# Optimization experiments

Hardware: AMD Instinct MI355X
Metric: run time of the kernel (lower is better)

The kernel has to match this reference:

```python
import jax, jax.numpy as jnp
import numpy as np

N, E = 100000, 1600000
F_IN, F_HID, F_OUT = 64, 64, 16


def setup_inputs() -> dict:
    key = jax.random.key(0)
    ks = jax.random.split(key, 10)
    def g(k, shape):
        return jax.random.normal(k, shape, dtype=jnp.float32) * 0.05
    return {
        "x": jax.random.normal(ks[0], (N, F_IN), dtype=jnp.float32),
        "adj": jax.random.randint(ks[1], (2, E), 0, N, dtype=jnp.int32),
        # ChebConv K=2 params: per-order weights [in, out] + shared bias
        "W1_0": g(ks[2], (F_IN, F_HID)), "W1_1": g(ks[3], (F_IN, F_HID)),
        "b1": jnp.zeros((F_HID,), jnp.float32),
        "Wx_0": g(ks[4], (F_HID, F_HID)), "Wx_1": g(ks[5], (F_HID, F_HID)),
        "bx": jnp.zeros((F_HID,), jnp.float32),
        "W2_0": g(ks[6], (F_HID, F_OUT)), "W2_1": g(ks[7], (F_HID, F_OUT)),
        "b2": jnp.zeros((F_OUT,), jnp.float32),
    }


def _cheb(x, row, col, w, W0, W1, b):
    # K=2 Chebyshev conv: Tx0 = x, Tx1 = L_hat @ x (sparse propagate)
    n = x.shape[0]
    tx1 = jax.ops.segment_sum(w[:, None] * x[col], row, num_segments=n)
    return x @ W0 + tx1 @ W1 + b


def reference(x, adj, W1_0, W1_1, b1, Wx_0, Wx_1, bx, W2_0, W2_1, b2):
    row, col = adj[0], adj[1]
    n = x.shape[0]
    # sym-normalized Laplacian scaled by 2/lambda_max (=1): diagonal cancels,
    # off-diagonal weight = -deg^{-1/2}[row] * deg^{-1/2}[col]
    deg = jax.ops.segment_sum(jnp.ones(adj.shape[1], x.dtype), row, num_segments=n)
    dis = jnp.where(deg > 0, jax.lax.rsqrt(jnp.maximum(deg, 1e-12)), 0.0)
    w = -dis[row] * dis[col]
    h = jax.nn.relu(_cheb(x, row, col, w, W1_0, W1_1, b1))
    # dropout is identity in eval mode
    h = jax.nn.relu(_cheb(h, row, col, w, Wx_0, Wx_1, bx))
    return _cheb(h, row, col, w, W2_0, W2_1, b2)
```

## Files before the change

kernel.cpp:

```cpp
#include <hip/hip_runtime.h>
#include <hip/hip_bf16.h>


#define EPB 4096

typedef __attribute__((ext_vector_type(8))) short bf16x8;
typedef __attribute__((ext_vector_type(4))) float f32x4;

__device__ __forceinline__ float bf2f(unsigned short u) {
    unsigned int x = ((unsigned int)u) << 16;
    return __uint_as_float(x);
}
__device__ __forceinline__ unsigned short f2bf(float f) {
    unsigned int b = __float_as_uint(f);
    unsigned int r = (b + 0x7FFF + ((b >> 16) & 1)) >> 16;
    return (unsigned short)r;
}

__global__ __launch_bounds__(256) void zero_ints(int* __restrict__ p, int n) {
    int i = blockIdx.x * 256 + threadIdx.x;
    if (i < n) p[i] = 0;
}

__global__ __launch_bounds__(256) void bucket_count(const int* __restrict__ row,
                                                    int* __restrict__ bcnt,
                                                    int e, int nbk) {
    __shared__ int bh[512];
    int tid = threadIdx.x;
    for (int j = tid; j < nbk; j += 256) bh[j] = 0;
    __syncthreads();
    int base = blockIdx.x * EPB;
#pragma unroll
    for (int k = 0; k < EPB / 256; ++k) {
        int i = base + k * 256 + tid;
        if (i < e) atomicAdd(&bh[row[i] >> 8], 1);
    }
    __syncthreads();
    for (int j = tid; j < nbk; j += 256) {
        int c = bh[j];
        if (c) atomicAdd(&bcnt[j], c);
    }
}

__global__ __launch_bounds__(256) void bucket_scan(const int* __restrict__ bcnt,
                                                   int* __restrict__ bbase,
                                                   int* __restrict__ bcursor,
                                                   int* __restrict__ off,
                                                   int nbk, int n, int e) {
    __shared__ int sa[512], sb[512];
    int tid = threadIdx.x;
    for (int j = tid; j < 512; j += 256) sa[j] = (j < nbk) ? bcnt[j] : 0;
    __syncthreads();
    int* in = sa;
    int* out = sb;
    for (int d = 1; d < 512; d <<= 1) {
        for (int j = tid; j < 512; j += 256)
            out[j] = in[j] + ((j >= d) ? in[j - d] : 0);
        __syncthreads();
        int* t = in; in = out; out = t;
    }
    for (int j = tid; j < nbk; j += 256) {
        int incl = in[j];
        int excl = incl - bcnt[j];
        bbase[j] = excl;
        bcursor[j] = excl;
        if (j == nbk - 1) bbase[nbk] = incl;
    }
    if (tid == 0) off[n] = e;
}

__global__ __launch_bounds__(256) void bucket_scatter(const int* __restrict__ row,
                                                      const int* __restrict__ col,
                                                      int* __restrict__ bcursor,
                                                      int* __restrict__ packed,
                                                      int e, int nbk) {
    __shared__ int bh[512];
    __shared__ int bbase[512];
    __shared__ int bcur[512];
    int tid = threadIdx.x;
    for (int j = tid; j < nbk; j += 256) { bh[j] = 0; bcur[j] = 0; }
    __syncthreads();
    int base = blockIdx.x * EPB;
#pragma unroll
    for (int k = 0; k < EPB / 256; ++k) {
        int i = base + k * 256 + tid;
        if (i < e) atomicAdd(&bh[row[i] >> 8], 1);
    }
    __syncthreads();
    for (int j = tid; j < nbk; j += 256) {
        int c = bh[j];
        bbase[j] = c ? atomicAdd(&bcursor[j], c) : 0;
    }
    __syncthreads();
#pragma unroll
    for (int k = 0; k < EPB / 256; ++k) {
        int i = base + k * 256 + tid;
        if (i < e) {
            int r = row[i];
            int b = r >> 8;
            int slot = bbase[b] + atomicAdd(&bcur[b], 1);
            packed[slot] = ((r & 255) << 17) | col[i];
        }
    }
}

__global__ __launch_bounds__(256) void bucket_build(const int* __restrict__ packed,
                                                    const int* __restrict__ bbase,
                                                    int* __restrict__ off,
                                                    float* __restrict__ dis,
                                                    int* __restrict__ csr, int n) {
    __shared__ int rcnt[256];
    __shared__ int sa[256], sb[256];
    int tid = threadIdx.x;
    int b = blockIdx.x;
    int ebase = bbase[b], eend = bbase[b + 1];
    rcnt[tid] = 0;
    __syncthreads();
    for (int e = ebase + tid; e < eend; e += 256)
        atomicAdd(&rcnt[packed[e] >> 17], 1);
    __syncthreads();
    sa[tid] = rcnt[tid];
    __syncthreads();
    int* in = sa;
    int* out = sb;
    for (int d = 1; d < 256; d <<= 1) {
        out[tid] = in[tid] + ((tid >= d) ? in[tid - d] : 0);
        __syncthreads();
        int* t = in; in = out; out = t;
    }
    int grow = b * 256 + tid;
    int c = rcnt[tid];
    int excl = in[tid] - c;
    if (grow < n) {
        off[grow] = ebase + excl;
        dis[grow] = (c > 0) ? rsqrtf((float)c) : 0.0f;
    }
    out[tid] = excl;
    __syncthreads();
    for (int e = ebase + tid; e < eend; e += 256) {
        int p = packed[e];
        int lr = p >> 17;
        int pos = atomicAdd(&out[lr], 1);
        csr[ebase + pos] = p & 0x1FFFF;
    }
}


__global__ __launch_bounds__(256) void scale_xy(const float* __restrict__ x,
                                                const float* __restrict__ dis,
                                                unsigned short* __restrict__ y,
                                                unsigned short* __restrict__ xb, int n) {
    int id = blockIdx.x * 256 + threadIdx.x;
    if (id < n * 16) {
        int r = id >> 4;
        float d = dis[r];
        float4 v = ((const float4*)x)[id];
        ushort4 o = {f2bf(v.x * d), f2bf(v.y * d), f2bf(v.z * d), f2bf(v.w * d)};
        ((ushort4*)y)[id] = o;
        ushort4 xo = {f2bf(v.x), f2bf(v.y), f2bf(v.z), f2bf(v.w)};
        ((ushort4*)xb)[id] = xo;
    }
}


__global__ __launch_bounds__(256) void aggregate(const unsigned short* __restrict__ y,
                                                 const int* __restrict__ csr,
                                                 const int* __restrict__ off,
                                                 const float* __restrict__ dis,
                                                 unsigned short* __restrict__ tx, int n) {
    int tid = threadIdx.x;
    int r = blockIdx.x * 16 + (tid >> 4);
    if (r >= n) return;
    int q = tid & 15;
    int s0 = off[r], e1 = off[r + 1];
    const ushort4* Y = (const ushort4*)y;
    float ax = 0.f, ay = 0.f, az = 0.f, aw = 0.f;
    int t = s0;
    for (; t + 8 <= e1; t += 8) {
        int c0 = csr[t], c1 = csr[t + 1], c2 = csr[t + 2], c3 = csr[t + 3];
        int c4 = csr[t + 4], c5 = csr[t + 5], c6 = csr[t + 6], c7 = csr[t + 7];
        ushort4 v0 = Y[(size_t)c0 * 16 + q];
        ushort4 v1 = Y[(size_t)c1 * 16 + q];
        ushort4 v2 = Y[(size_t)c2 * 16 + q];
        ushort4 v3 = Y[(size_t)c3 * 16 + q];
        ushort4 v4 = Y[(size_t)c4 * 16 + q];
        ushort4 v5 = Y[(size_t)c5 * 16 + q];
        ushort4 v6 = Y[(size_t)c6 * 16 + q];
        ushort4 v7 = Y[(size_t)c7 * 16 + q];
        ax += ((bf2f(v0.x) + bf2f(v1.x)) + (bf2f(v2.x) + bf2f(v3.x))) +
              ((bf2f(v4.x) + bf2f(v5.x)) + (bf2f(v6.x) + bf2f(v7.x)));
        ay += ((bf2f(v0.y) + bf2f(v1.y)) + (bf2f(v2.y) + bf2f(v3.y))) +
              ((bf2f(v4.y) + bf2f(v5.y)) + (bf2f(v6.y) + bf2f(v7.y)));
        az += ((bf2f(v0.z) + bf2f(v1.z)) + (bf2f(v2.z) + bf2f(v3.z))) +
              ((bf2f(v4.z) + bf2f(v5.z)) + (bf2f(v6.z) + bf2f(v7.z)));
        aw += ((bf2f(v0.w) + bf2f(v1.w)) + (bf2f(v2.w) + bf2f(v3.w))) +
              ((bf2f(v4.w) + bf2f(v5.w)) + (bf2f(v6.w) + bf2f(v7.w)));
    }
    for (; t + 4 <= e1; t += 4) {
        int c0 = csr[t], c1 = csr[t + 1], c2 = csr[t + 2], c3 = csr[t + 3];
        ushort4 v0 = Y[(size_t)c0 * 16 + q];
        ushort4 v1 = Y[(size_t)c1 * 16 + q];
        ushort4 v2 = Y[(size_t)c2 * 16 + q];
        ushort4 v3 = Y[(size_t)c3 * 16 + q];
        ax += (bf2f(v0.x) + bf2f(v1.x)) + (bf2f(v2.x) + bf2f(v3.x));
        ay += (bf2f(v0.y) + bf2f(v1.y)) + (bf2f(v2.y) + bf2f(v3.y));
        az += (bf2f(v0.z) + bf2f(v1.z)) + (bf2f(v2.z) + bf2f(v3.z));
        aw += (bf2f(v0.w) + bf2f(v1.w)) + (bf2f(v2.w) + bf2f(v3.w));
    }
    for (; t < e1; ++t) {
        int c = csr[t];
        ushort4 v = Y[(size_t)c * 16 + q];
        ax += bf2f(v.x); ay += bf2f(v.y); az += bf2f(v.z); aw += bf2f(v.w);
    }
    float d = -dis[r];
    ushort4 o = {f2bf(ax * d), f2bf(ay * d), f2bf(az * d), f2bf(aw * d)};
    *(ushort4*)&tx[(size_t)r * 64 + q * 4] = o;
}


template <int NC, bool RELU, bool WRITE_HY>
__global__ __launch_bounds__(256) void dense_mfma(const unsigned short* __restrict__ A0,
                                                  const unsigned short* __restrict__ A1,
                                                  const float* __restrict__ W0,
                                                  const float* __restrict__ W1,
                                                  const float* __restrict__ bias,
                                                  const float* __restrict__ dis,
                                                  unsigned short* __restrict__ hout,
                                                  unsigned short* __restrict__ yout,
                                                  float* __restrict__ fout,
                                                  int n, int nrb) {
    constexpr int NT = NC / 16;
    int lane = threadIdx.x & 63;
    int m = lane & 15;
    int g = lane >> 4;
    bf16x8 bf[NT][4];
#pragma unroll
    for (int kt = 0; kt < 4; ++kt) {
        const float* W = (kt < 2) ? W0 : W1;
        int kb = (kt & 1) * 32 + g * 8;
#pragma unroll
        for (int nt = 0; nt < NT; ++nt) {
#pragma unroll
            for (int i = 0; i < 8; ++i)
                bf[nt][kt][i] = (short)f2bf(W[(kb + i) * NC + nt * 16 + m]);
        }
    }
    int wrb = blockIdx.x * 4 + (threadIdx.x >> 6);
    int stride = gridDim.x * 4;
    for (int rb = wrb; rb < nrb; rb += stride) {
        int r0 = rb * 16;
        int ra = r0 + m;
        if (ra > n - 1) ra = n - 1;
        const unsigned short* q0 = A0 + (size_t)ra * 64 + g * 8;
        const unsigned short* q1 = A1 + (size_t)ra * 64 + g * 8;
        bf16x8 a0 = *(const bf16x8*)q0;
        bf16x8 a1 = *(const bf16x8*)(q0 + 32);
        bf16x8 a2 = *(const bf16x8*)q1;
        bf16x8 a3 = *(const bf16x8*)(q1 + 32);
        f32x4 acc[NT];
#pragma unroll
        for (int nt = 0; nt < NT; ++nt) {
            float b = bias[nt * 16 + m];
            acc[nt][0] = b; acc[nt][1] = b; acc[nt][2] = b; acc[nt][3] = b;
        }
#pragma unroll
        for (int nt = 0; nt < NT; ++nt) {
            acc[nt] = __builtin_amdgcn_mfma_f32_16x16x32_bf16(a0, bf[nt][0], acc[nt], 0, 0, 0);
            acc[nt] = __builtin_amdgcn_mfma_f32_16x16x32_bf16(a1, bf[nt][1], acc[nt], 0, 0, 0);
            acc[nt] = __builtin_amdgcn_mfma_f32_16x16x32_bf16(a2, bf[nt][2], acc[nt], 0, 0, 0);
            acc[nt] = __builtin_amdgcn_mfma_f32_16x16x32_bf16(a3, bf[nt][3], acc[nt], 0, 0, 0);
        }
#pragma unroll
        for (int reg = 0; reg < 4; ++reg) {
            int rr = r0 + 4 * g + reg;
            if (rr >= n) continue;
            if (WRITE_HY) {
                float dv = dis[rr];
#pragma unroll
                for (int nt = 0; nt < NT; ++nt) {
                    float v = acc[nt][reg];
                    if (RELU) v = fmaxf(v, 0.f);
                    hout[(size_t)rr * NC + nt * 16 + m] = f2bf(v);
                    yout[(size_t)rr * NC + nt * 16 + m] = f2bf(v * dv);
                }
            } else {
#pragma unroll
                for (int nt = 0; nt < NT; ++nt)
                    fout[(size_t)rr * NC + nt * 16 + m] = acc[nt][reg];
            }
        }
    }
}


extern "C" void kernel_launch(void* const* d_in, const int* in_sizes, int n_in,
                              void* d_out, int out_size, void* d_ws, size_t ws_size,
                              hipStream_t stream) {
    const float* x    = (const float*)d_in[0];
    const int*   adj  = (const int*)d_in[1];
    const float* W1_0 = (const float*)d_in[2];
    const float* W1_1 = (const float*)d_in[3];
    const float* b1   = (const float*)d_in[4];
    const float* Wx_0 = (const float*)d_in[5];
    const float* Wx_1 = (const float*)d_in[6];
    const float* bx   = (const float*)d_in[7];
    const float* W2_0 = (const float*)d_in[8];
    const float* W2_1 = (const float*)d_in[9];
    const float* b2   = (const float*)d_in[10];
    float* out = (float*)d_out;

    int N = in_sizes[0] / 64;
    int E = in_sizes[1] / 2;
    const int* row = adj;
    const int* col = adj + E;
    int NBK = (N + 255) / 256;
    int nRB = (N + 15) / 16;

    char* p = (char*)d_ws;
    auto alloc = [&](size_t bytes) {
        char* q = p;
        p += (bytes + 255) & ~(size_t)255;
        return q;
    };
    int*   bcnt  = (int*)alloc((size_t)(NBK) * 4);
    int*   bbase = (int*)alloc((size_t)(NBK + 1) * 4);
    int*   bcur  = (int*)alloc((size_t)(NBK) * 4);
    int*   off   = (int*)alloc((size_t)(N + 1) * 4);
    float* dis   = (float*)alloc((size_t)N * 4);
    int*   csr   = (int*)alloc((size_t)E * 4);
    unsigned short* y  = (unsigned short*)alloc((size_t)N * 64 * 2);
    unsigned short* xb = (unsigned short*)alloc((size_t)N * 64 * 2);
    unsigned short* tx = (unsigned short*)alloc((size_t)N * 64 * 2);
    unsigned short* h  = (unsigned short*)alloc((size_t)N * 64 * 2);
    (void)ws_size;
    int* packed = (int*)tx;

    int EB = (E + EPB - 1) / EPB;
    zero_ints<<<(NBK + 255) / 256, 256, 0, stream>>>(bcnt, NBK);
    bucket_count<<<EB, 256, 0, stream>>>(row, bcnt, E, NBK);
    bucket_scan<<<1, 256, 0, stream>>>(bcnt, bbase, bcur, off, NBK, N, E);
    bucket_scatter<<<EB, 256, 0, stream>>>(row, col, bcur, packed, E, NBK);
    bucket_build<<<NBK, 256, 0, stream>>>(packed, bbase, off, dis, csr, N);

    const int DG = 512;
    scale_xy<<<(N * 16 + 255) / 256, 256, 0, stream>>>(x, dis, y, xb, N);
    aggregate<<<(N + 15) / 16, 256, 0, stream>>>(y, csr, off, dis, tx, N);
    dense_mfma<64, true, true><<<DG, 256, 0, stream>>>(xb, tx, W1_0, W1_1, b1, dis, h, y, nullptr, N, nRB);
    aggregate<<<(N + 15) / 16, 256, 0, stream>>>(y, csr, off, dis, tx, N);
    dense_mfma<64, true, true><<<DG, 256, 0, stream>>>(h, tx, Wx_0, Wx_1, bx, dis, h, y, nullptr, N, nRB);
    aggregate<<<(N + 15) / 16, 256, 0, stream>>>(y, csr, off, dis, tx, N);
    dense_mfma<16, false, false><<<DG, 256, 0, stream>>>(h, tx, W2_0, W2_1, b2, dis, nullptr, nullptr, out, N, nRB);
}
```

Before: 203.5 us.

## Fuse x scaling into CSR build and prepack weights to bf16 once

Folds the former scale_xy kernel into bucket_build, so each block scales and converts its 256 rows of x using degree-inverse-sqrt values kept in shared memory, which removes one launch. A new wconv_all kernel converts all six weight matrices to bf16 in MFMA fragment order up front, so each dense_mfma wave does vector loads instead of strided fp32 loads plus conversion per block. The cost is one extra small launch and more work in the tail of bucket_build, where 391 blocks may give less parallelism for the x pass than the old fully parallel kernel.

```diff
diff --git a/kernel.cpp b/kernel.cpp
--- a/kernel.cpp
+++ b/kernel.cpp
@@ -20,6 +20,37 @@
 __global__ __launch_bounds__(256) void zero_ints(int* __restrict__ p, int n) {
     int i = blockIdx.x * 256 + threadIdx.x;
     if (i < n) p[i] = 0;
+}
+
+template <int NC>
+__device__ __forceinline__ void pack_pair(const float* __restrict__ W0,
+                                          const float* __restrict__ W1,
+                                          unsigned short* __restrict__ out, int idx) {
+    constexpr int NT = NC / 16;
+    int i = idx & 7;
+    int m = (idx >> 3) & 15;
+    int g = (idx >> 7) & 3;
+    int f = idx >> 9;
+    int nt = f % NT;
+    int kt = f / NT;
+    const float* W = (kt < 2) ? W0 : W1;
+    int k = (kt & 1) * 32 + g * 8 + i;
+    out[idx] = f2bf(W[k * NC + nt * 16 + m]);
+}
+
+__global__ __launch_bounds__(256) void wconv_all(const float* __restrict__ W1_0,
+                                                 const float* __restrict__ W1_1,
+                                                 const float* __restrict__ Wx_0,
+                                                 const float* __restrict__ Wx_1,
+                                                 const float* __restrict__ W2_0,
+                                                 const float* __restrict__ W2_1,
+                                                 unsigned short* __restrict__ wp1,
+                                                 unsigned short* __restrict__ wpx,
+                                                 unsigned short* __restrict__ wp2) {
+    int idx = blockIdx.x * 256 + threadIdx.x;
+    if (idx < 8192) pack_pair<64>(W1_0, W1_1, wp1, idx);
+    else if (idx < 16384) pack_pair<64>(Wx_0, Wx_1, wpx, idx - 8192);
+    else if (idx < 18432) pack_pair<16>(W2_0, W2_1, wp2, idx - 16384);
 }
 
 __global__ __launch_bounds__(256) void bucket_count(const int* __restrict__ row,
@@ -106,11 +137,16 @@
 
 __global__ __launch_bounds__(256) void bucket_build(const int* __restrict__ packed,
                                                     const int* __restrict__ bbase,
+                                                    const float* __restrict__ x,
                                                     int* __restrict__ off,
                                                     float* __restrict__ dis,
-                                                    int* __restrict__ csr, int n) {
+                                                    int* __restrict__ csr,
+                                                    unsigned short* __restrict__ y,
+                                                    unsigned short* __restrict__ xb,
+                                                    int n) {
     __shared__ int rcnt[256];
     __shared__ int sa[256], sb[256];
+    __shared__ float disv[256];
     int tid = threadIdx.x;
     int b = blockIdx.x;
     int ebase = bbase[b], eend = bbase[b + 1];
@@ -131,9 +167,11 @@
     int grow = b * 256 + tid;
     int c = rcnt[tid];
     int excl = in[tid] - c;
+    float dv = (c > 0) ? rsqrtf((float)c) : 0.0f;
+    disv[tid] = dv;
     if (grow < n) {
         off[grow] = ebase + excl;
-        dis[grow] = (c > 0) ? rsqrtf((float)c) : 0.0f;
+        dis[grow] = dv;
     }
     out[tid] = excl;
     __syncthreads();
@@ -143,22 +181,17 @@
         int pos = atomicAdd(&out[lr], 1);
         csr[ebase + pos] = p & 0x1FFFF;
     }
-}
-
-
-__global__ __launch_bounds__(256) void scale_xy(const float* __restrict__ x,
-                                                const float* __restrict__ dis,
-                                                unsigned short* __restrict__ y,
-                                                unsigned short* __restrict__ xb, int n) {
-    int id = blockIdx.x * 256 + threadIdx.x;
-    if (id < n * 16) {
-        int r = id >> 4;
-        float d = dis[r];
-        float4 v = ((const float4*)x)[id];
-        ushort4 o = {f2bf(v.x * d), f2bf(v.y * d), f2bf(v.z * d), f2bf(v.w * d)};
-        ((ushort4*)y)[id] = o;
-        ushort4 xo = {f2bf(v.x), f2bf(v.y), f2bf(v.z), f2bf(v.w)};
-        ((ushort4*)xb)[id] = xo;
+    for (int idx = tid; idx < 4096; idx += 256) {
+        int rr = idx >> 4, q = idx & 15;
+        int R = b * 256 + rr;
+        if (R < n) {
+            float d = disv[rr];
+            float4 v = ((const float4*)x)[(size_t)R * 16 + q];
+            ushort4 o = {f2bf(v.x * d), f2bf(v.y * d), f2bf(v.z * d), f2bf(v.w * d)};
+            ((ushort4*)y)[(size_t)R * 16 + q] = o;
+            ushort4 xo = {f2bf(v.x), f2bf(v.y), f2bf(v.z), f2bf(v.w)};
+            ((ushort4*)xb)[(size_t)R * 16 + q] = xo;
+        }
     }
 }
 
@@ -221,8 +254,7 @@
 template <int NC, bool RELU, bool WRITE_HY>
 __global__ __launch_bounds__(256) void dense_mfma(const unsigned short* __restrict__ A0,
                                                   const unsigned short* __restrict__ A1,
-                                                  const float* __restrict__ W0,
-                                                  const float* __restrict__ W1,
+                                                  const unsigned short* __restrict__ Wp,
                                                   const float* __restrict__ bias,
                                                   const float* __restrict__ dis,
                                                   unsigned short* __restrict__ hout,
@@ -233,18 +265,13 @@
     int lane = threadIdx.x & 63;
     int m = lane & 15;
     int g = lane >> 4;
+    const bf16x8* WP = (const bf16x8*)Wp;
     bf16x8 bf[NT][4];
 #pragma unroll
-    for (int kt = 0; kt < 4; ++kt) {
-        const float* W = (kt < 2) ? W0 : W1;
-        int kb = (kt & 1) * 32 + g * 8;
-#pragma unroll
-        for (int nt = 0; nt < NT; ++nt) {
-#pragma unroll
-            for (int i = 0; i < 8; ++i)
-                bf[nt][kt][i] = (short)f2bf(W[(kb + i) * NC + nt * 16 + m]);
-        }
-    }
+    for (int kt = 0; kt < 4; ++kt)
+#pragma unroll
+        for (int nt = 0; nt < NT; ++nt)
+            bf[nt][kt] = WP[((kt * NT + nt) * 4 + g) * 16 + m];
     int wrb = blockIdx.x * 4 + (threadIdx.x >> 6);
     int stride = gridDim.x * 4;
     for (int rb = wrb; rb < nrb; rb += stride) {
@@ -328,6 +355,9 @@
     int*   off   = (int*)alloc((size_t)(N + 1) * 4);
     float* dis   = (float*)alloc((size_t)N * 4);
     int*   csr   = (int*)alloc((size_t)E * 4);
+    unsigned short* wp1 = (unsigned short*)alloc(8192 * 2);
+    unsigned short* wpx = (unsigned short*)alloc(8192 * 2);
+    unsigned short* wp2 = (unsigned short*)alloc(2048 * 2);
     unsigned short* y  = (unsigned short*)alloc((size_t)N * 64 * 2);
     unsigned short* xb = (unsigned short*)alloc((size_t)N * 64 * 2);
     unsigned short* tx = (unsigned short*)alloc((size_t)N * 64 * 2);
@@ -337,17 +367,17 @@
 
     int EB = (E + EPB - 1) / EPB;
     zero_ints<<<(NBK + 255) / 256, 256, 0, stream>>>(bcnt, NBK);
+    wconv_all<<<72, 256, 0, stream>>>(W1_0, W1_1, Wx_0, Wx_1, W2_0, W2_1, wp1, wpx, wp2);
     bucket_count<<<EB, 256, 0, stream>>>(row, bcnt, E, NBK);
     bucket_scan<<<1, 256, 0, stream>>>(bcnt, bbase, bcur, off, NBK, N, E);
     bucket_scatter<<<EB, 256, 0, stream>>>(row, col, bcur, packed, E, NBK);
-    bucket_build<<<NBK, 256, 0, stream>>>(packed, bbase, off, dis, csr, N);
+    bucket_build<<<NBK, 256, 0, stream>>>(packed, bbase, x, off, dis, csr, y, xb, N);
 
     const int DG = 512;
-    scale_xy<<<(N * 16 + 255) / 256, 256, 0, stream>>>(x, dis, y, xb, N);
     aggregate<<<(N + 15) / 16, 256, 0, stream>>>(y, csr, off, dis, tx, N);
-    dense_mfma<64, true, true><<<DG, 256, 0, stream>>>(xb, tx, W1_0, W1_1, b1, dis, h, y, nullptr, N, nRB);
+    dense_mfma<64, true, true><<<DG, 256, 0, stream>>>(xb, tx, wp1, b1, dis, h, y, nullptr, N, nRB);
     aggregate<<<(N + 15) / 16, 256, 0, stream>>>(y, csr, off, dis, tx, N);
-    dense_mfma<64, true, true><<<DG, 256, 0, stream>>>(h, tx, Wx_0, Wx_1, bx, dis, h, y, nullptr, N, nRB);
+    dense_mfma<64, true, true><<<DG, 256, 0, stream>>>(h, tx, wpx, bx, dis, h, y, nullptr, N, nRB);
     aggregate<<<(N + 15) / 16, 256, 0, stream>>>(y, csr, off, dis, tx, N);
-    dense_mfma<16, false, false><<<DG, 256, 0, stream>>>(h, tx, W2_0, W2_1, b2, dis, nullptr, nullptr, out, N, nRB);
-}
+    dense_mfma<16, false, false><<<DG, 256, 0, stream>>>(h, tx, wp2, b2, dis, nullptr, nullptr, out, N, nRB);
+}
```

New measurement: 202.7 us. No clear change (-0.4%).
